# Optimization experiments

Measured on AMD Instinct MI355X. Metric: run time of the kernel, lower is better.

## Reference

```python
import jax, jax.numpy as jnp
import numpy as np

N = 10000       # nodes
E = 160000      # edges (avg degree 16)
IN_C = 16       # node in_channels
IN_E = 8        # edge in_edge_channels
DIMS = [32, 16, 16, 16]   # hidden_dims
ENN_H = 128     # edge_nn_hidden
EMLP_H = 16     # edge_mlp_hidden


def setup_inputs() -> dict:
    key = jax.random.key(0)
    ks = iter(jax.random.split(key, 80))
    def rn(shape, s=0.1):
        return jax.random.normal(next(ks), shape, dtype=jnp.float32) * s
    inp = {}
    inp['x'] = jax.random.normal(next(ks), (N, IN_C), dtype=jnp.float32)
    inp['edge_attr'] = jax.random.normal(next(ks), (E, IN_E), dtype=jnp.float32)
    inp['edge_index'] = jax.random.randint(next(ks), (2, E), 0, N, dtype=jnp.int32)
    in_dims = [IN_C] + DIMS[:-1]
    for i, (di, do) in enumerate(zip(in_dims, DIMS)):
        inp[f'p_w{i}'] = rn((do, di));            inp[f'p_b{i}'] = rn((do,))
        inp[f'e1_w{i}'] = rn((ENN_H, IN_E));      inp[f'e1_b{i}'] = rn((ENN_H,))
        inp[f'e2_w{i}'] = rn((do * do, ENN_H), 0.02); inp[f'e2_b{i}'] = rn((do * do,), 0.02)
        inp[f'r_w{i}'] = rn((do, do));            inp[f'c_b{i}'] = rn((do,))
    inp['m_w0'] = rn((EMLP_H, DIMS[-1])); inp['m_b0'] = rn((EMLP_H,))
    inp['m_w1'] = rn((1, EMLP_H));        inp['m_b1'] = rn((1,))
    return inp


def _forward(x, edge_attr, edge_index, params, m_w0, m_b0, m_w1, m_b1):
    row, col = edge_index[0], edge_index[1]
    n = x.shape[0]
    # in-degree for scatter-mean (clamped to 1, as PyG scatter mean)
    deg = jnp.clip(jax.ops.segment_sum(jnp.ones(row.shape[0], jnp.float32), col, num_segments=n), 1.0)
    for (pw, pb, ew1, eb1, ew2, eb2, rw, cb) in params:
        d = pw.shape[0]
        x_proj = x @ pw.T + pb                                    # [N, d]
        # edge-conditioned weight matrices: [E, d, d]
        W = (jax.nn.relu(edge_attr @ ew1.T + eb1) @ ew2.T + eb2).reshape(-1, d, d)
        msg = jnp.einsum('ei,eio->eo', x_proj[row], W)            # [E, d]
        agg = jax.ops.segment_sum(msg, col, num_segments=n) / deg[:, None]
        conv = agg + x_proj @ rw.T + cb                           # NNConv: aggr + root + bias
        x = jax.nn.relu(conv) + x_proj                            # relu + skip
    edge_repr = x[row] + x[col]                                   # [E, d_last]
    out = jax.nn.relu(edge_repr @ m_w0.T + m_b0) @ m_w1.T + m_b1  # [E, 1]
    return out[:, 0]


def reference(x, edge_attr, edge_index,
              p_w0, p_b0, e1_w0, e1_b0, e2_w0, e2_b0, r_w0, c_b0,
              p_w1, p_b1, e1_w1, e1_b1, e2_w1, e2_b1, r_w1, c_b1,
              p_w2, p_b2, e1_w2, e1_b2, e2_w2, e2_b2, r_w2, c_b2,
              p_w3, p_b3, e1_w3, e1_b3, e2_w3, e2_b3, r_w3, c_b3,
              m_w0, m_b0, m_w1, m_b1):
    params = [
        (p_w0, p_b0, e1_w0, e1_b0, e2_w0, e2_b0, r_w0, c_b0),
        (p_w1, p_b1, e1_w1, e1_b1, e2_w1, e2_b1, r_w1, c_b1),
        (p_w2, p_b2, e1_w2, e1_b2, e2_w2, e2_b2, r_w2, c_b2),
        (p_w3, p_b3, e1_w3, e1_b3, e2_w3, e2_b3, r_w3, c_b3),
    ]
    return _forward(x, edge_attr, edge_index, params, m_w0, m_b0, m_w1, m_b1)
```

## Files before the change

kernel.cpp:

```cpp
#include <hip/hip_runtime.h>

#define NN 10000
#define NE 160000
static constexpr int TPB = 256;
static constexpr int SCAN_T = 1024;

typedef unsigned int uint32;

static __device__ __forceinline__ ushort f2bf(float f) {
  uint32 u = __float_as_uint(f);
  u += 0x7fff + ((u >> 16) & 1);
  return (ushort)(u >> 16);
}
static __device__ __forceinline__ uint32 pk2bf(float a, float b) {
  return (uint32)f2bf(a) | ((uint32)f2bf(b) << 16);
}
static __device__ __forceinline__ float bflo(uint32 u) {
  return __uint_as_float(u << 16);
}
static __device__ __forceinline__ float bfhi(uint32 u) {
  return __uint_as_float(u & 0xffff0000u);
}
static __device__ __forceinline__ void dot2bf(float& acc, uint32 a, uint32 b) {
  asm("v_dot2_f32_bf16 %0, %1, %2, %0" : "+v"(acc) : "v"(a), "v"(b));
}


__global__ void k_count(const int* __restrict__ ei, int* __restrict__ cnt) {
  int e = blockIdx.x * TPB + threadIdx.x;
  if (e >= NE) return;
  atomicAdd(&cnt[ei[e]], 1);
  atomicAdd(&cnt[NN + ei[NE + e]], 1);
}

__global__ void __launch_bounds__(SCAN_T)
k_scan2(const int* __restrict__ cnt_all, int* __restrict__ off_r, int* __restrict__ cur_r,
        int* __restrict__ off_c, int* __restrict__ cur_c) {
  const int* cnt = (blockIdx.x == 0) ? cnt_all : cnt_all + NN;
  int* off = (blockIdx.x == 0) ? off_r : off_c;
  int* cur = (blockIdx.x == 0) ? cur_r : cur_c;
  __shared__ int s_wave[16];
  __shared__ int s_carry;
  int tid = threadIdx.x;
  int lane = tid & 63, wid = tid >> 6;
  if (tid == 0) s_carry = 0;
  __syncthreads();
  for (int base = 0; base < NN; base += SCAN_T) {
    int i = base + tid;
    int v = (i < NN) ? cnt[i] : 0;
    int s = v;
    #pragma unroll
    for (int d = 1; d < 64; d <<= 1) {
      int t = __shfl_up(s, d, 64);
      if (lane >= d) s += t;
    }
    if (lane == 63) s_wave[wid] = s;
    __syncthreads();
    if (wid == 0 && lane < 16) {
      int ws = s_wave[lane];
      #pragma unroll
      for (int d = 1; d < 16; d <<= 1) {
        int t = __shfl_up(ws, d, 64);
        if (lane >= d) ws += t;
      }
      s_wave[lane] = ws;
    }
    __syncthreads();
    int waveoff = (wid > 0) ? s_wave[wid - 1] : 0;
    int excl = s_carry + waveoff + s - v;
    if (i < NN) { off[i] = excl; cur[i] = excl; }
    __syncthreads();
    if (tid == 0) s_carry += s_wave[15];
    __syncthreads();
  }
  if (tid == 0) off[NN] = s_carry;
}

__global__ void k_fill_row(const int* __restrict__ ei, int* __restrict__ cur_row,
                           int* __restrict__ eid_row) {
  int e = blockIdx.x * TPB + threadIdx.x;
  if (e >= NE) return;
  int r = ei[e];
  int p = atomicAdd(&cur_row[r], 1);
  eid_row[p] = e;
}

__global__ void k_fill_colpos(const int* __restrict__ ei, const int* __restrict__ eid_row,
                              int* __restrict__ cur_col, int* __restrict__ colpos) {
  int s = blockIdx.x * TPB + threadIdx.x;
  if (s >= NE) return;
  int e = eid_row[s];
  int c = ei[NE + e];
  int p = atomicAdd(&cur_col[c], 1);
  colpos[s] = p;
}


template<int DIN, int D>
__global__ void __launch_bounds__(TPB)
k_nodeprep(const float* __restrict__ x, const float* __restrict__ pw, const float* __restrict__ pb,
           const float* __restrict__ rw, const float* __restrict__ cb, const float* __restrict__ eb2,
           float* __restrict__ xp, float* __restrict__ root, float* __restrict__ Bb) {
  __shared__ float s_pw[D * DIN], s_rw[D * D], s_eb2[D * D], s_pb[D], s_cb[D];
  for (int t = threadIdx.x; t < D * DIN; t += TPB) s_pw[t] = pw[t];
  for (int t = threadIdx.x; t < D * D; t += TPB) { s_rw[t] = rw[t]; s_eb2[t] = eb2[t]; }
  for (int t = threadIdx.x; t < D; t += TPB) { s_pb[t] = pb[t]; s_cb[t] = cb[t]; }
  __syncthreads();
  int n = blockIdx.x * TPB + threadIdx.x;
  if (n >= NN) return;
  float xv[DIN];
  const float4* x4 = (const float4*)(x + (size_t)n * DIN);
  #pragma unroll
  for (int i = 0; i < DIN / 4; i++) {
    float4 v = x4[i];
    xv[4*i+0] = v.x; xv[4*i+1] = v.y; xv[4*i+2] = v.z; xv[4*i+3] = v.w;
  }
  float xpv[D];
  #pragma unroll
  for (int o = 0; o < D; o++) {
    float a = s_pb[o];
    #pragma unroll
    for (int i = 0; i < DIN; i++) a = fmaf(s_pw[o*DIN + i], xv[i], a);
    xpv[o] = a;
    xp[(size_t)n*D + o] = a;
  }
  #pragma unroll
  for (int o = 0; o < D; o++) {
    float a = s_cb[o];
    #pragma unroll
    for (int i = 0; i < D; i++) a = fmaf(s_rw[o*D + i], xpv[i], a);
    root[(size_t)n*D + o] = a;
  }
  #pragma unroll
  for (int o = 0; o < D; o++) {
    float a = 0.f;
    #pragma unroll
    for (int i = 0; i < D; i++) a = fmaf(xpv[i], s_eb2[i*D + o], a);
    Bb[(size_t)n*D + o] = a;
  }
}

template<int DP, int D>
__global__ void __launch_bounds__(TPB)
k_aggprep(const int* __restrict__ col_off,
          const uint32* __restrict__ msg0p, const uint32* __restrict__ msg1p,
          const float* __restrict__ root_prev, const float* __restrict__ xp_prev,
          const float* __restrict__ pw, const float* __restrict__ pb,
          const float* __restrict__ rw, const float* __restrict__ cb,
          const float* __restrict__ eb2,
          float* __restrict__ xp, float* __restrict__ root, float* __restrict__ Bb) {
  constexpr int W = DP / 2;
  constexpr int NB = TPB / W;
  __shared__ float s_x[NB][DP];
  __shared__ float s_xpv[NB][D];
  __shared__ float s_pw[D * DP], s_rw[D * D], s_eb2[D * D], s_pb[D], s_cb[D];
  int tid = threadIdx.x;
  for (int t = tid; t < D * DP; t += TPB) s_pw[t] = pw[t];
  for (int t = tid; t < D * D; t += TPB) { s_rw[t] = rw[t]; s_eb2[t] = eb2[t]; }
  for (int t = tid; t < D; t += TPB) { s_pb[t] = pb[t]; s_cb[t] = cb[t]; }
  int g = tid / W, o2 = tid % W;
  int n = blockIdx.x * NB + g;
  if (n < NN) {
    int p0 = col_off[n], p1 = col_off[n + 1];
    float ax = 0.f, ay = 0.f;
    for (int p = p0; p < p1; p++) {
      uint32 w0 = msg0p[(size_t)p * W + o2];
      uint32 w1 = msg1p[(size_t)p * W + o2];
      ax += bflo(w0) + bflo(w1);
      ay += bfhi(w0) + bfhi(w1);
    }
    float deg = (p1 > p0) ? (float)(p1 - p0) : 1.f;
    float2 rp = *(const float2*)(root_prev + (size_t)n * DP + 2 * o2);
    float2 xq = *(const float2*)(xp_prev + (size_t)n * DP + 2 * o2);
    float c0 = ax / deg + rp.x, c1 = ay / deg + rp.y;
    s_x[g][2 * o2]     = (c0 > 0.f ? c0 : 0.f) + xq.x;
    s_x[g][2 * o2 + 1] = (c1 > 0.f ? c1 : 0.f) + xq.y;
  }
  __syncthreads();
  for (int t = tid; t < NB * D; t += TPB) {
    int g2 = t / D, o = t % D;
    int n2 = blockIdx.x * NB + g2;
    if (n2 < NN) {
      float a = s_pb[o];
      #pragma unroll
      for (int i = 0; i < DP; i++) a = fmaf(s_pw[o * DP + i], s_x[g2][i], a);
      s_xpv[g2][o] = a;
      xp[(size_t)n2 * D + o] = a;
    }
  }
  __syncthreads();
  for (int t = tid; t < NB * D; t += TPB) {
    int g2 = t / D, o = t % D;
    int n2 = blockIdx.x * NB + g2;
    if (n2 < NN) {
      float r2 = s_cb[o], b2 = 0.f;
      #pragma unroll
      for (int i = 0; i < D; i++) {
        r2 = fmaf(s_rw[o * D + i], s_xpv[g2][i], r2);
        b2 = fmaf(s_xpv[g2][i], s_eb2[i * D + o], b2);
      }
      root[(size_t)n2 * D + o] = r2;
      Bb[(size_t)n2 * D + o] = b2;
    }
  }
}

__global__ void k_trans_all(const float* __restrict__ e0, const float* __restrict__ e1,
                            const float* __restrict__ e2, const float* __restrict__ e3,
                            uint32* __restrict__ Vp) {
  int t = blockIdx.x * TPB + threadIdx.x;
  const float* ew2; uint32* dst; int D, loc;
  if (t < 65536)       { ew2 = e0; dst = Vp;         D = 32; loc = t; }
  else if (t < 81920)  { ew2 = e1; dst = Vp + 65536; D = 16; loc = t - 65536; }
  else if (t < 98304)  { ew2 = e2; dst = Vp + 81920; D = 16; loc = t - 81920; }
  else if (t < 114688) { ew2 = e3; dst = Vp + 98304; D = 16; loc = t - 98304; }
  else return;
  int COLS = D * 128;
  int i2 = loc / COLS;
  int r = loc - i2 * COLS;
  int w = r >> 1, p = r & 1;
  int k2 = w / D, o = w - k2 * D;
  int k = 2 * k2 + p;
  float lo = ew2[((size_t)((2 * i2) * D + o)) * 128 + k];
  float hi = ew2[((size_t)((2 * i2 + 1) * D + o)) * 128 + k];
  dst[loc] = pk2bf(lo, hi);
}

template<int D, int G>
__global__ void __launch_bounds__(TPB)
k_fused(const int* __restrict__ eid_row, const int* __restrict__ row_off,
        const int* __restrict__ colpos,
        const float* __restrict__ ea, const float* __restrict__ ew1,
        const float* __restrict__ eb1, const uint32* __restrict__ Vp,
        const float* __restrict__ xp, const float* __restrict__ Bb,
        uint32* __restrict__ msg0p, uint32* __restrict__ msg1p) {
  constexpr int OQ = D / 4;
  constexpr int EB = TPB / OQ;
  constexpr int COLS = D * 128;
  constexpr int UW = COLS / 2;
  constexpr int UH = UW / 2;
  constexpr int UP = UH + 4;
  constexpr int CT = UH / TPB;

  __shared__ __align__(16) uint32 s_w1tp[4 * 64];
  __shared__ float  s_b1[64];
  __shared__ __align__(16) uint32 s_U[G * UP];
  __shared__ __align__(16) uint32 s_hp[EB * 36];
  __shared__ __align__(16) uint32 s_eap[EB * 4];
  __shared__ int    s_cp[EB];
  __shared__ uint32 s_xp2[G][D / 2];
  __shared__ float  s_B[G * D];
  __shared__ int    s_off[G + 1];

  int tid = threadIdx.x;
  int half = blockIdx.y;
  int n0 = blockIdx.x * G;
  int GA = NN - n0; if (GA > G) GA = G;
  uint32* msgHp = half ? msg1p : msg0p;

  for (int t = tid; t < 4 * 64; t += TPB) {
    int i2 = t >> 6, kloc = t & 63;
    int k = half * 64 + kloc;
    s_w1tp[t] = pk2bf(ew1[k * 8 + 2 * i2], ew1[k * 8 + 2 * i2 + 1]);
  }
  for (int t = tid; t < 64; t += TPB) s_b1[t] = eb1[half * 64 + t];
  for (int t = tid; t < G * (D / 2); t += TPB) {
    int g = t / (D / 2), i2 = t % (D / 2);
    if (g < GA) {
      float2 v = *(const float2*)(xp + (size_t)(n0 + g) * D + 2 * i2);
      s_xp2[g][i2] = pk2bf(v.x, v.y);
    } else {
      s_xp2[g][i2] = 0;
    }
  }
  for (int t = tid; t < G * D; t += TPB) {
    int g = t / D, i = t % D;
    s_B[t] = (g < GA && half == 0) ? Bb[(size_t)(n0 + g) * D + i] : 0.f;
  }
  if (tid <= GA) s_off[tid] = row_off[n0 + tid];
  __syncthreads();

  {
    const uint2* Vp2 = (const uint2*)Vp;
    float accLo[G][CT], accHi[G][CT];
    #pragma unroll
    for (int g = 0; g < G; g++)
      #pragma unroll
      for (int j = 0; j < CT; j++) { accLo[g][j] = 0.f; accHi[g][j] = 0.f; }
    #pragma unroll 2
    for (int i2 = 0; i2 < D / 2; i2++) {
      uint2 vv[CT];
      #pragma unroll
      for (int j = 0; j < CT; j++)
        vv[j] = Vp2[(size_t)i2 * UW + half * UH + j * TPB + tid];
      #pragma unroll
      for (int g = 0; g < G; g++) {
        uint32 xg = s_xp2[g][i2];
        #pragma unroll
        for (int j = 0; j < CT; j++) {
          dot2bf(accLo[g][j], xg, vv[j].x);
          dot2bf(accHi[g][j], xg, vv[j].y);
        }
      }
    }
    #pragma unroll
    for (int g = 0; g < G; g++)
      #pragma unroll
      for (int j = 0; j < CT; j++)
        s_U[g * UP + j * TPB + tid] = pk2bf(accLo[g][j], accHi[g][j]);
  }

  int p0 = row_off[n0], p1 = row_off[n0 + GA];
  int el = tid / OQ, oq = tid % OQ;
  for (int pc = p0; pc < p1; pc += EB) {
    int cnt = p1 - pc; if (cnt > EB) cnt = EB;
    __syncthreads();
    for (int t = tid; t < cnt * 4; t += TPB) {
      int e2 = t >> 2, i2 = t & 3;
      float2 v = *(const float2*)(ea + (size_t)eid_row[pc + e2] * 8 + 2 * i2);
      s_eap[t] = pk2bf(v.x, v.y);
    }
    for (int t = tid; t < cnt; t += TPB) s_cp[t] = colpos[pc + t];
    __syncthreads();
    for (int t = tid; t < cnt * 32; t += TPB) {
      int e2 = t >> 5, k2 = t & 31;
      float a0 = s_b1[2 * k2], a1 = s_b1[2 * k2 + 1];
      #pragma unroll
      for (int i2 = 0; i2 < 4; i2++) {
        uint32 ep = s_eap[e2 * 4 + i2];
        uint2 ww = *(const uint2*)(s_w1tp + i2 * 64 + 2 * k2);
        dot2bf(a0, ep, ww.x);
        dot2bf(a1, ep, ww.y);
      }
      s_hp[e2 * 36 + k2] = pk2bf(fmaxf(a0, 0.f), fmaxf(a1, 0.f));
    }
    __syncthreads();
    if (el < cnt) {
      int g = 0;
      {
        int s = pc + el;
        #pragma unroll
        for (int q = 1; q < G; q++) g += (q < GA && s >= s_off[q]) ? 1 : 0;
      }
      const uint32* up = s_U + g * UP + oq * 4;
      const uint32* hp = s_hp + el * 36;
      float a0 = 0.f, a1 = 0.f, a2 = 0.f, a3 = 0.f;
      #pragma unroll
      for (int k8 = 0; k8 < 8; k8++) {
        uint4 hw = *(const uint4*)(hp + 4 * k8);
        uint4 u0 = *(const uint4*)(up + (4 * k8 + 0) * D);
        uint4 u1 = *(const uint4*)(up + (4 * k8 + 1) * D);
        uint4 u2 = *(const uint4*)(up + (4 * k8 + 2) * D);
        uint4 u3 = *(const uint4*)(up + (4 * k8 + 3) * D);
        dot2bf(a0, hw.x, u0.x); dot2bf(a1, hw.x, u0.y); dot2bf(a2, hw.x, u0.z); dot2bf(a3, hw.x, u0.w);
        dot2bf(a0, hw.y, u1.x); dot2bf(a1, hw.y, u1.y); dot2bf(a2, hw.y, u1.z); dot2bf(a3, hw.y, u1.w);
        dot2bf(a0, hw.z, u2.x); dot2bf(a1, hw.z, u2.y); dot2bf(a2, hw.z, u2.z); dot2bf(a3, hw.z, u2.w);
        dot2bf(a0, hw.w, u3.x); dot2bf(a1, hw.w, u3.y); dot2bf(a2, hw.w, u3.z); dot2bf(a3, hw.w, u3.w);
      }
      float4 b = ((const float4*)(s_B + g * D))[oq];
      uint2 om;
      om.x = pk2bf(a0 + b.x, a1 + b.y);
      om.y = pk2bf(a2 + b.z, a3 + b.w);
      ((uint2*)(msgHp + (size_t)s_cp[el] * (D / 2)))[oq] = om;
    }
  }
}

template<int D>
__global__ void __launch_bounds__(TPB)
k_agg(const int* __restrict__ col_off,
      const uint32* __restrict__ msg0p, const uint32* __restrict__ msg1p,
      const float* __restrict__ root, const float* __restrict__ xp,
      float* __restrict__ xout) {
  constexpr int W = D / 2;
  constexpr int GP = TPB / W;
  int g = threadIdx.x / W, o2 = threadIdx.x % W;
  int n = blockIdx.x * GP + g;
  if (n >= NN) return;
  int p0 = col_off[n], p1 = col_off[n + 1];
  float ax = 0.f, ay = 0.f;
  for (int p = p0; p < p1; p++) {
    uint32 w0 = msg0p[(size_t)p * W + o2];
    uint32 w1 = msg1p[(size_t)p * W + o2];
    ax += bflo(w0) + bflo(w1);
    ay += bfhi(w0) + bfhi(w1);
  }
  float deg = (p1 > p0) ? (float)(p1 - p0) : 1.f;
  float2 rp = *(const float2*)(root + (size_t)n * D + 2 * o2);
  float2 xq = *(const float2*)(xp + (size_t)n * D + 2 * o2);
  float c0 = ax / deg + rp.x, c1 = ay / deg + rp.y;
  xout[(size_t)n * D + 2 * o2]     = (c0 > 0.f ? c0 : 0.f) + xq.x;
  xout[(size_t)n * D + 2 * o2 + 1] = (c1 > 0.f ? c1 : 0.f) + xq.y;
}

__global__ void __launch_bounds__(TPB)
k_final(const int* __restrict__ ei, const float* __restrict__ x,
        const float* __restrict__ mw0, const float* __restrict__ mb0,
        const float* __restrict__ mw1, const float* __restrict__ mb1,
        float* __restrict__ out) {
  __shared__ float s_w0[256], s_b0[16], s_w1[16], s_b1;
  for (int t = threadIdx.x; t < 256; t += TPB) s_w0[t] = mw0[t];
  if (threadIdx.x < 16) { s_b0[threadIdx.x] = mb0[threadIdx.x]; s_w1[threadIdx.x] = mw1[threadIdx.x]; }
  if (threadIdx.x == 0) s_b1 = mb1[0];
  __syncthreads();
  int e = blockIdx.x * TPB + threadIdx.x;
  if (e >= NE) return;
  int r = ei[e], c = ei[NE + e];
  const float4* xr4 = (const float4*)(x + (size_t)r * 16);
  const float4* xc4 = (const float4*)(x + (size_t)c * 16);
  float er[16];
  #pragma unroll
  for (int q = 0; q < 4; q++) {
    float4 vr = xr4[q], vc = xc4[q];
    er[4*q+0] = vr.x + vc.x; er[4*q+1] = vr.y + vc.y;
    er[4*q+2] = vr.z + vc.z; er[4*q+3] = vr.w + vc.w;
  }
  float o = s_b1;
  #pragma unroll
  for (int j = 0; j < 16; j++) {
    float t = s_b0[j];
    #pragma unroll
    for (int k = 0; k < 16; k++) t = fmaf(er[k], s_w0[j * 16 + k], t);
    t = fmaxf(t, 0.f);
    o = fmaf(t, s_w1[j], o);
  }
  out[e] = o;
}


struct LayerPtrs {
  const float *pw, *pb, *ew1, *eb1, *ew2, *eb2, *rw, *cb;
};

extern "C" void kernel_launch(void* const* d_in, const int* in_sizes, int n_in,
                              void* d_out, int out_size, void* d_ws, size_t ws_size,
                              hipStream_t stream) {
  (void)in_sizes; (void)n_in; (void)out_size; (void)ws_size;
  const float* x0 = (const float*)d_in[0];
  const float* ea = (const float*)d_in[1];
  const int* ei = (const int*)d_in[2];
  LayerPtrs L[4];
  for (int l = 0; l < 4; l++) {
    L[l].pw  = (const float*)d_in[3 + 8 * l];
    L[l].pb  = (const float*)d_in[4 + 8 * l];
    L[l].ew1 = (const float*)d_in[5 + 8 * l];
    L[l].eb1 = (const float*)d_in[6 + 8 * l];
    L[l].ew2 = (const float*)d_in[7 + 8 * l];
    L[l].eb2 = (const float*)d_in[8 + 8 * l];
    L[l].rw  = (const float*)d_in[9 + 8 * l];
    L[l].cb  = (const float*)d_in[10 + 8 * l];
  }
  const float* mw0 = (const float*)d_in[35];
  const float* mb0 = (const float*)d_in[36];
  const float* mw1 = (const float*)d_in[37];
  const float* mb1 = (const float*)d_in[38];
  float* out = (float*)d_out;

  char* w = (char*)d_ws;
  size_t off = 0;
  auto alloc = [&](size_t b) -> void* {
    void* p = w + off;
    off = (off + b + 255) & ~(size_t)255;
    return p;
  };
  int* cnt      = (int*)alloc(sizeof(int) * 2 * NN);
  int* row_off  = (int*)alloc(sizeof(int) * (NN + 1));
  int* col_off  = (int*)alloc(sizeof(int) * (NN + 1));
  int* cur_row  = (int*)alloc(sizeof(int) * NN);
  int* cur_col  = (int*)alloc(sizeof(int) * NN);
  int* eid_row  = (int*)alloc(sizeof(int) * NE);
  int* colpos   = (int*)alloc(sizeof(int) * NE);
  float* xpA   = (float*)alloc(sizeof(float) * NN * 32);
  float* xpB   = (float*)alloc(sizeof(float) * NN * 32);
  float* rootA = (float*)alloc(sizeof(float) * NN * 32);
  float* rootB = (float*)alloc(sizeof(float) * NN * 32);
  float* Bb    = (float*)alloc(sizeof(float) * NN * 32);
  uint32* msg0p = (uint32*)alloc(sizeof(uint32) * NE * 16);
  uint32* msg1p = (uint32*)alloc(sizeof(uint32) * NE * 16);
  float* xfin  = (float*)alloc(sizeof(float) * NN * 16);
  uint32* Vp   = (uint32*)alloc(sizeof(uint32) * 114688);

  hipMemsetAsync(cnt, 0, sizeof(int) * 2 * NN, stream);
  k_count<<<(NE + TPB - 1) / TPB, TPB, 0, stream>>>(ei, cnt);
  k_scan2<<<2, SCAN_T, 0, stream>>>(cnt, row_off, cur_row, col_off, cur_col);
  k_fill_row<<<(NE + TPB - 1) / TPB, TPB, 0, stream>>>(ei, cur_row, eid_row);
  k_fill_colpos<<<(NE + TPB - 1) / TPB, TPB, 0, stream>>>(ei, eid_row, cur_col, colpos);
  k_trans_all<<<(114688 + TPB - 1) / TPB, TPB, 0, stream>>>(
      L[0].ew2, L[1].ew2, L[2].ew2, L[3].ew2, Vp);

  k_nodeprep<16, 32><<<(NN + TPB - 1) / TPB, TPB, 0, stream>>>(
      x0, L[0].pw, L[0].pb, L[0].rw, L[0].cb, L[0].eb2, xpA, rootA, Bb);
  {
    dim3 gf((NN + 5) / 6, 2);
    k_fused<32, 6><<<gf, TPB, 0, stream>>>(
        eid_row, row_off, colpos, ea, L[0].ew1, L[0].eb1, Vp, xpA, Bb, msg0p, msg1p);
  }
  k_aggprep<32, 16><<<(NN + 15) / 16, TPB, 0, stream>>>(
      col_off, msg0p, msg1p, rootA, xpA,
      L[1].pw, L[1].pb, L[1].rw, L[1].cb, L[1].eb2, xpB, rootB, Bb);
  {
    dim3 gf((NN + 5) / 6, 2);
    k_fused<16, 6><<<gf, TPB, 0, stream>>>(
        eid_row, row_off, colpos, ea, L[1].ew1, L[1].eb1, Vp + 65536, xpB, Bb, msg0p, msg1p);
  }
  k_aggprep<16, 16><<<(NN + 31) / 32, TPB, 0, stream>>>(
      col_off, msg0p, msg1p, rootB, xpB,
      L[2].pw, L[2].pb, L[2].rw, L[2].cb, L[2].eb2, xpA, rootA, Bb);
  {
    dim3 gf((NN + 5) / 6, 2);
    k_fused<16, 6><<<gf, TPB, 0, stream>>>(
        eid_row, row_off, colpos, ea, L[2].ew1, L[2].eb1, Vp + 81920, xpA, Bb, msg0p, msg1p);
  }
  k_aggprep<16, 16><<<(NN + 31) / 32, TPB, 0, stream>>>(
      col_off, msg0p, msg1p, rootA, xpA,
      L[3].pw, L[3].pb, L[3].rw, L[3].cb, L[3].eb2, xpB, rootB, Bb);
  {
    dim3 gf((NN + 5) / 6, 2);
    k_fused<16, 6><<<gf, TPB, 0, stream>>>(
        eid_row, row_off, colpos, ea, L[3].ew1, L[3].eb1, Vp + 98304, xpB, Bb, msg0p, msg1p);
  }
  k_agg<16><<<(NN + 31) / 32, TPB, 0, stream>>>(
      col_off, msg0p, msg1p, rootB, xpB, xfin);
  k_final<<<(NE + TPB - 1) / TPB, TPB, 0, stream>>>(ei, xfin, mw0, mb0, mw1, mb1, out);
}
```

Measured before the change: 298.0 us.

## Pair edges per thread in fused edge kernel to reuse U loads

The fused edge kernel now groups the edges of each source node into pairs, building a per-block pair table in shared memory. Each thread computes two edge messages, so each set of U values read from shared memory serves two dot products and LDS traffic per edge drops. The D=16 layers also go from 6 to 4 nodes per block, trading more blocks and more per-block U precompute for less LDS per block. Risks include wasted work on odd-degree nodes, a serial prefix loop on thread 0, and the MAXP cap of 256 pairs, which could silently drop edges for high-degree groups.

```diff
diff --git a/kernel.cpp b/kernel.cpp
--- a/kernel.cpp
+++ b/kernel.cpp
@@ -6,6 +6,7 @@
 static constexpr int SCAN_T = 1024;
 
 typedef unsigned int uint32;
+typedef unsigned char uchar;
 
 static __device__ __forceinline__ ushort f2bf(float f) {
   uint32 u = __float_as_uint(f);
@@ -235,22 +236,28 @@
         const float* __restrict__ xp, const float* __restrict__ Bb,
         uint32* __restrict__ msg0p, uint32* __restrict__ msg1p) {
   constexpr int OQ = D / 4;
-  constexpr int EB = TPB / OQ;
+  constexpr int EBP = TPB / OQ;
   constexpr int COLS = D * 128;
   constexpr int UW = COLS / 2;
   constexpr int UH = UW / 2;
   constexpr int UP = UH + 4;
   constexpr int CT = UH / TPB;
+  constexpr int HSTR = 36;
+  constexpr int MAXP = 256;
 
   __shared__ __align__(16) uint32 s_w1tp[4 * 64];
   __shared__ float  s_b1[64];
   __shared__ __align__(16) uint32 s_U[G * UP];
-  __shared__ __align__(16) uint32 s_hp[EB * 36];
-  __shared__ __align__(16) uint32 s_eap[EB * 4];
-  __shared__ int    s_cp[EB];
+  __shared__ __align__(16) uint32 s_hp[(2 * EBP + 1) * HSTR];
+  __shared__ __align__(16) uint32 s_eap[(2 * EBP + 2) * 4];
+  __shared__ int    s_cp[2 * EBP + 2];
   __shared__ uint32 s_xp2[G][D / 2];
   __shared__ float  s_B[G * D];
   __shared__ int    s_off[G + 1];
+  __shared__ int    s_pbase[G + 1];
+  __shared__ int    s_np;
+  __shared__ int    s_pe[MAXP];
+  __shared__ uchar  s_pg[MAXP];
 
   int tid = threadIdx.x;
   int half = blockIdx.y;
@@ -278,6 +285,30 @@
     s_B[t] = (g < GA && half == 0) ? Bb[(size_t)(n0 + g) * D + i] : 0.f;
   }
   if (tid <= GA) s_off[tid] = row_off[n0 + tid];
+  if (tid == 0) {
+    int acc = 0;
+    int prev = row_off[n0];
+    for (int g = 0; g < GA; g++) {
+      s_pbase[g] = acc;
+      int nx = row_off[n0 + g + 1];
+      acc += (nx - prev + 1) >> 1;
+      prev = nx;
+    }
+    s_np = (acc > MAXP) ? MAXP : acc;
+  }
+  __syncthreads();
+
+  int np = s_np;
+  for (int t = tid; t < np; t += TPB) {
+    int g = 0;
+    #pragma unroll
+    for (int q = 1; q < G; q++) g += (q < GA && t >= s_pbase[q]) ? 1 : 0;
+    int j = t - s_pbase[g];
+    int base = s_off[g];
+    int deg = s_off[g + 1] - base;
+    s_pe[t] = base + 2 * j;
+    s_pg[t] = (uchar)(g | (((2 * j + 1) < deg) ? 8 : 0));
+  }
   __syncthreads();
 
   {
@@ -310,19 +341,21 @@
         s_U[g * UP + j * TPB + tid] = pk2bf(accLo[g][j], accHi[g][j]);
   }
 
-  int p0 = row_off[n0], p1 = row_off[n0 + GA];
-  int el = tid / OQ, oq = tid % OQ;
-  for (int pc = p0; pc < p1; pc += EB) {
-    int cnt = p1 - pc; if (cnt > EB) cnt = EB;
-    __syncthreads();
-    for (int t = tid; t < cnt * 4; t += TPB) {
+  for (int pp = 0; pp < np; pp += EBP) {
+    int cntp = np - pp; if (cntp > EBP) cntp = EBP;
+    int eF = s_pe[pp];
+    int plast = pp + cntp - 1;
+    int eL = s_pe[plast] + ((s_pg[plast] & 8) ? 2 : 1);
+    int cnte = eL - eF;
+    __syncthreads();
+    for (int t = tid; t < cnte * 4; t += TPB) {
       int e2 = t >> 2, i2 = t & 3;
-      float2 v = *(const float2*)(ea + (size_t)eid_row[pc + e2] * 8 + 2 * i2);
+      float2 v = *(const float2*)(ea + (size_t)eid_row[eF + e2] * 8 + 2 * i2);
       s_eap[t] = pk2bf(v.x, v.y);
     }
-    for (int t = tid; t < cnt; t += TPB) s_cp[t] = colpos[pc + t];
-    __syncthreads();
-    for (int t = tid; t < cnt * 32; t += TPB) {
+    for (int t = tid; t < cnte; t += TPB) s_cp[t] = colpos[eF + t];
+    __syncthreads();
+    for (int t = tid; t < cnte * 32; t += TPB) {
       int e2 = t >> 5, k2 = t & 31;
       float a0 = s_b1[2 * k2], a1 = s_b1[2 * k2 + 1];
       #pragma unroll
@@ -332,36 +365,50 @@
         dot2bf(a0, ep, ww.x);
         dot2bf(a1, ep, ww.y);
       }
-      s_hp[e2 * 36 + k2] = pk2bf(fmaxf(a0, 0.f), fmaxf(a1, 0.f));
-    }
-    __syncthreads();
-    if (el < cnt) {
-      int g = 0;
-      {
-        int s = pc + el;
-        #pragma unroll
-        for (int q = 1; q < G; q++) g += (q < GA && s >= s_off[q]) ? 1 : 0;
-      }
+      s_hp[e2 * HSTR + k2] = pk2bf(fmaxf(a0, 0.f), fmaxf(a1, 0.f));
+    }
+    __syncthreads();
+    int pi = tid / OQ, oq = tid % OQ;
+    if (pi < cntp) {
+      int pidx = pp + pi;
+      int e0 = s_pe[pidx];
+      uchar gz = s_pg[pidx];
+      int g = gz & 7;
+      int two = gz >> 3;
+      int el0 = e0 - eF;
       const uint32* up = s_U + g * UP + oq * 4;
-      const uint32* hp = s_hp + el * 36;
+      const uint32* hA = s_hp + el0 * HSTR;
+      const uint32* hB = hA + HSTR;
       float a0 = 0.f, a1 = 0.f, a2 = 0.f, a3 = 0.f;
+      float b0 = 0.f, b1 = 0.f, b2 = 0.f, b3 = 0.f;
       #pragma unroll
       for (int k8 = 0; k8 < 8; k8++) {
-        uint4 hw = *(const uint4*)(hp + 4 * k8);
+        uint4 hwA = *(const uint4*)(hA + 4 * k8);
+        uint4 hwB = *(const uint4*)(hB + 4 * k8);
         uint4 u0 = *(const uint4*)(up + (4 * k8 + 0) * D);
         uint4 u1 = *(const uint4*)(up + (4 * k8 + 1) * D);
         uint4 u2 = *(const uint4*)(up + (4 * k8 + 2) * D);
         uint4 u3 = *(const uint4*)(up + (4 * k8 + 3) * D);
-        dot2bf(a0, hw.x, u0.x); dot2bf(a1, hw.x, u0.y); dot2bf(a2, hw.x, u0.z); dot2bf(a3, hw.x, u0.w);
-        dot2bf(a0, hw.y, u1.x); dot2bf(a1, hw.y, u1.y); dot2bf(a2, hw.y, u1.z); dot2bf(a3, hw.y, u1.w);
-        dot2bf(a0, hw.z, u2.x); dot2bf(a1, hw.z, u2.y); dot2bf(a2, hw.z, u2.z); dot2bf(a3, hw.z, u2.w);
-        dot2bf(a0, hw.w, u3.x); dot2bf(a1, hw.w, u3.y); dot2bf(a2, hw.w, u3.z); dot2bf(a3, hw.w, u3.w);
+        dot2bf(a0, hwA.x, u0.x); dot2bf(a1, hwA.x, u0.y); dot2bf(a2, hwA.x, u0.z); dot2bf(a3, hwA.x, u0.w);
+        dot2bf(a0, hwA.y, u1.x); dot2bf(a1, hwA.y, u1.y); dot2bf(a2, hwA.y, u1.z); dot2bf(a3, hwA.y, u1.w);
+        dot2bf(a0, hwA.z, u2.x); dot2bf(a1, hwA.z, u2.y); dot2bf(a2, hwA.z, u2.z); dot2bf(a3, hwA.z, u2.w);
+        dot2bf(a0, hwA.w, u3.x); dot2bf(a1, hwA.w, u3.y); dot2bf(a2, hwA.w, u3.z); dot2bf(a3, hwA.w, u3.w);
+        dot2bf(b0, hwB.x, u0.x); dot2bf(b1, hwB.x, u0.y); dot2bf(b2, hwB.x, u0.z); dot2bf(b3, hwB.x, u0.w);
+        dot2bf(b0, hwB.y, u1.x); dot2bf(b1, hwB.y, u1.y); dot2bf(b2, hwB.y, u1.z); dot2bf(b3, hwB.y, u1.w);
+        dot2bf(b0, hwB.z, u2.x); dot2bf(b1, hwB.z, u2.y); dot2bf(b2, hwB.z, u2.z); dot2bf(b3, hwB.z, u2.w);
+        dot2bf(b0, hwB.w, u3.x); dot2bf(b1, hwB.w, u3.y); dot2bf(b2, hwB.w, u3.z); dot2bf(b3, hwB.w, u3.w);
       }
-      float4 b = ((const float4*)(s_B + g * D))[oq];
-      uint2 om;
-      om.x = pk2bf(a0 + b.x, a1 + b.y);
-      om.y = pk2bf(a2 + b.z, a3 + b.w);
-      ((uint2*)(msgHp + (size_t)s_cp[el] * (D / 2)))[oq] = om;
+      float4 bb = ((const float4*)(s_B + g * D))[oq];
+      uint2 omA;
+      omA.x = pk2bf(a0 + bb.x, a1 + bb.y);
+      omA.y = pk2bf(a2 + bb.z, a3 + bb.w);
+      ((uint2*)(msgHp + (size_t)s_cp[el0] * (D / 2)))[oq] = omA;
+      if (two) {
+        uint2 omB;
+        omB.x = pk2bf(b0 + bb.x, b1 + bb.y);
+        omB.y = pk2bf(b2 + bb.z, b3 + bb.w);
+        ((uint2*)(msgHp + (size_t)s_cp[el0 + 1] * (D / 2)))[oq] = omB;
+      }
     }
   }
 }
@@ -499,24 +546,24 @@
       col_off, msg0p, msg1p, rootA, xpA,
       L[1].pw, L[1].pb, L[1].rw, L[1].cb, L[1].eb2, xpB, rootB, Bb);
   {
-    dim3 gf((NN + 5) / 6, 2);
-    k_fused<16, 6><<<gf, TPB, 0, stream>>>(
+    dim3 gf((NN + 3) / 4, 2);
+    k_fused<16, 4><<<gf, TPB, 0, stream>>>(
         eid_row, row_off, colpos, ea, L[1].ew1, L[1].eb1, Vp + 65536, xpB, Bb, msg0p, msg1p);
   }
   k_aggprep<16, 16><<<(NN + 31) / 32, TPB, 0, stream>>>(
       col_off, msg0p, msg1p, rootB, xpB,
       L[2].pw, L[2].pb, L[2].rw, L[2].cb, L[2].eb2, xpA, rootA, Bb);
   {
-    dim3 gf((NN + 5) / 6, 2);
-    k_fused<16, 6><<<gf, TPB, 0, stream>>>(
+    dim3 gf((NN + 3) / 4, 2);
+    k_fused<16, 4><<<gf, TPB, 0, stream>>>(
         eid_row, row_off, colpos, ea, L[2].ew1, L[2].eb1, Vp + 81920, xpA, Bb, msg0p, msg1p);
   }
   k_aggprep<16, 16><<<(NN + 31) / 32, TPB, 0, stream>>>(
       col_off, msg0p, msg1p, rootA, xpA,
       L[3].pw, L[3].pb, L[3].rw, L[3].cb, L[3].eb2, xpB, rootB, Bb);
   {
-    dim3 gf((NN + 5) / 6, 2);
-    k_fused<16, 6><<<gf, TPB, 0, stream>>>(
+    dim3 gf((NN + 3) / 4, 2);
+    k_fused<16, 4><<<gf, TPB, 0, stream>>>(
         eid_row, row_off, colpos, ea, L[3].ew1, L[3].eb1, Vp + 98304, xpB, Bb, msg0p, msg1p);
   }
   k_agg<16><<<(NN + 31) / 32, TPB, 0, stream>>>(
```

Result: slower. 334.1 us (+12.1%).
